# Performance work log

Measured on AMD Instinct MI355X. Metric: run time of the kernel, lower is better.

Reference implementation:

```python
import jax, jax.numpy as jnp
import numpy as np

N_NODES = 50000
N_EDGES = 800000
N_GRAPHS = 1000
IN_CH = 78
HID = 128
EPS = 1e-5


def _mean_aggr(x, src, dst, n):
    # scatter-mean of source-node features onto destination nodes
    s = jax.ops.segment_sum(x[src], dst, num_segments=n)
    deg = jax.ops.segment_sum(jnp.ones((src.shape[0],), x.dtype), dst, num_segments=n)
    return s / jnp.maximum(deg, 1.0)[:, None]


def _sage(x, src, dst, W_n, b_n, W_r):
    # PyG SAGEConv (mean): lin_l(mean_j x_j) + lin_r(x_i); lin_l has bias
    agg = _mean_aggr(x, src, dst, x.shape[0])
    return agg @ W_n + b_n + x @ W_r


def _bn(x, gamma, beta):
    # training-mode BatchNorm1d over node dimension (biased variance)
    mu = jnp.mean(x, axis=0)
    var = jnp.mean((x - mu) ** 2, axis=0)
    return (x - mu) * jax.lax.rsqrt(var + EPS) * gamma + beta


def setup_inputs() -> dict:
    key = jax.random.key(0)
    ks = jax.random.split(key, 20)
    d = {}
    d["x"] = jax.random.normal(ks[0], (N_NODES, IN_CH), dtype=jnp.float32)
    d["edge_index"] = jax.random.randint(ks[1], (2, N_EDGES), 0, N_NODES, dtype=jnp.int64)
    d["batch"] = jnp.sort(jax.random.randint(ks[2], (N_NODES,), 0, N_GRAPHS, dtype=jnp.int64))
    dims = [(IN_CH, HID), (HID, HID), (HID, HID)]
    for i, (di, do) in enumerate(dims):
        d[f"W_n{i}"] = jax.random.normal(ks[3 + 4 * i], (di, do), dtype=jnp.float32) * 0.05
        d[f"b{i}"] = jnp.zeros((do,), dtype=jnp.float32)
        d[f"W_r{i}"] = jax.random.normal(ks[4 + 4 * i], (di, do), dtype=jnp.float32) * 0.05
        d[f"g{i}"] = jnp.ones((do,), dtype=jnp.float32)
        d[f"be{i}"] = jnp.zeros((do,), dtype=jnp.float32)
    d["Wh1"] = jax.random.normal(ks[16], (HID, HID // 2), dtype=jnp.float32) * 0.05
    d["bh1"] = jnp.zeros((HID // 2,), dtype=jnp.float32)
    d["Wh2"] = jax.random.normal(ks[17], (HID // 2, 1), dtype=jnp.float32) * 0.05
    d["bh2"] = jnp.zeros((1,), dtype=jnp.float32)
    return d


def reference(x, edge_index, batch,
              W_n0, b0, W_r0, g0, be0,
              W_n1, b1, W_r1, g1, be1,
              W_n2, b2, W_r2, g2, be2,
              Wh1, bh1, Wh2, bh2):
    src, dst = edge_index[0], edge_index[1]
    layers = [(W_n0, b0, W_r0, g0, be0), (W_n1, b1, W_r1, g1, be1), (W_n2, b2, W_r2, g2, be2)]
    h = x
    for W_n, b_n, W_r, gamma, beta in layers:
        h = jax.nn.relu(_bn(_sage(h, src, dst, W_n, b_n, W_r), gamma, beta))
    # global mean pool per graph: [N_GRAPHS, HID]
    s = jax.ops.segment_sum(h, batch, num_segments=N_GRAPHS)
    cnt = jax.ops.segment_sum(jnp.ones((h.shape[0],), h.dtype), batch, num_segments=N_GRAPHS)
    pooled = s / jnp.maximum(cnt, 1.0)[:, None]
    return jax.nn.relu(pooled @ Wh1 + bh1) @ Wh2 + bh2
```

## Files before the change

kernel.cpp:

```cpp
#include <hip/hip_runtime.h>
#include <hip/hip_bf16.h>
#include <math.h>

#define HID 128
#define NSB 128
#define NBLK_BIN 256
#define BINC_CAP 6144

typedef short short8 __attribute__((ext_vector_type(8)));
typedef float f32x4 __attribute__((ext_vector_type(4)));

__global__ void prep_kernel(const float* __restrict__ x, float* __restrict__ xp,
                            int* __restrict__ bcnt, int nbuck16,
                            float* __restrict__ pstats, int npstats,
                            const float* __restrict__ Wn0, const float* __restrict__ Wr0,
                            const float* __restrict__ Wn1, const float* __restrict__ Wr1,
                            const float* __restrict__ Wn2, const float* __restrict__ Wr2,
                            unsigned short* __restrict__ B0h, unsigned short* __restrict__ B0l,
                            unsigned short* __restrict__ B1h, unsigned short* __restrict__ B1l,
                            unsigned short* __restrict__ B2h, unsigned short* __restrict__ B2l,
                            int N, int K0, int K0pad) {
    int i = blockIdx.x * blockDim.x + threadIdx.x;
    if (i < nbuck16) bcnt[i] = 0;
    if (i < npstats) pstats[i] = 0.f;
    if (i < N * K0pad) {
        int row = i / K0pad;
        int c = i - row * K0pad;
        xp[i] = (c < K0) ? x[(size_t)row * K0 + c] : 0.f;
    }
    int n0 = 256 * K0pad, n1 = 256 * HID;
    if (i < n0 + 2 * n1) {
        const float *Wn, *Wr;
        unsigned short *bh, *bl;
        int K, idx;
        if (i < n0) { Wn = Wn0; Wr = Wr0; bh = B0h; bl = B0l; K = K0; idx = i; }
        else if (i < n0 + n1) { Wn = Wn1; Wr = Wr1; bh = B1h; bl = B1l; K = HID; idx = i - n0; }
        else { Wn = Wn2; Wr = Wr2; bh = B2h; bl = B2l; K = HID; idx = i - n0 - n1; }
        int j = idx & 7;
        int lane = (idx >> 3) & 63;
        int cb = (idx >> 9) & 15;
        int ks = idx >> 13;
        int k = ks * 32 + ((lane >> 4) & 3) * 8 + j;
        int ch = 16 * cb + (lane & 15);
        float v = 0.f;
        if (k < K) v = (ch < 128) ? Wn[k * 128 + ch] : Wr[k * 128 + (ch - 128)];
        __hip_bfloat16 h = __float2bfloat16(v);
        float hf = __bfloat162float(h);
        __hip_bfloat16 l = __float2bfloat16(v - hf);
        bh[idx] = *(unsigned short*)&h;
        bl[idx] = *(unsigned short*)&l;
    }
}

__global__ void binA_kernel(const int* __restrict__ dst, int* __restrict__ bcnt,
                            int ne, int nbuck, int shift) {
    __shared__ int hist[512];
    int t = threadIdx.x;
    for (int i = t; i < 512; i += 256) hist[i] = 0;
    __syncthreads();
    size_t beg = (size_t)ne * blockIdx.x / NBLK_BIN;
    size_t end = (size_t)ne * (blockIdx.x + 1) / NBLK_BIN;
    for (size_t e = beg + t; e < end; e += 256)
        atomicAdd(&hist[dst[e] >> shift], 1);
    __syncthreads();
    for (int b = t; b < nbuck; b += 256) {
        int h = hist[b];
        if (h) atomicAdd(&bcnt[b * 16], h);
    }
}

__global__ __launch_bounds__(512) void bucket_scan_kernel(const int* __restrict__ bcnt,
                                                          int* __restrict__ bbase,
                                                          int* __restrict__ bcur, int nbuck) {
    __shared__ int tmp[512];
    int t = threadIdx.x;
    int v = (t < nbuck) ? bcnt[t * 16] : 0;
    tmp[t] = v;
    __syncthreads();
    for (int off = 1; off < 512; off <<= 1) {
        int u = 0;
        if (t >= off) u = tmp[t - off];
        __syncthreads();
        if (t >= off) tmp[t] += u;
        __syncthreads();
    }
    if (t < nbuck) {
        int exc = tmp[t] - v;
        bbase[t] = exc;
        bcur[t * 16] = exc;
        if (t == nbuck - 1) bbase[nbuck] = tmp[t];
    }
}

__global__ void binB_kernel(const int* __restrict__ src, const int* __restrict__ dst,
                            int* __restrict__ bcur, uint2* __restrict__ ebuf,
                            int ne, int nbuck, int shift) {
    __shared__ int hist[512];
    __shared__ int base[512];
    int t = threadIdx.x;
    for (int i = t; i < 512; i += 256) hist[i] = 0;
    __syncthreads();
    size_t beg = (size_t)ne * blockIdx.x / NBLK_BIN;
    size_t end = (size_t)ne * (blockIdx.x + 1) / NBLK_BIN;
    for (size_t e = beg + t; e < end; e += 256)
        atomicAdd(&hist[dst[e] >> shift], 1);
    __syncthreads();
    for (int b = t; b < nbuck; b += 256) {
        int h = hist[b];
        if (h) base[b] = atomicAdd(&bcur[b * 16], h);
        hist[b] = 0;
    }
    __syncthreads();
    for (size_t e = beg + t; e < end; e += 256) {
        int d = dst[e];
        int bk = d >> shift;
        int r = atomicAdd(&hist[bk], 1);
        ebuf[base[bk] + r] = make_uint2((unsigned)src[e], (unsigned)d);
    }
}

__global__ __launch_bounds__(512) void binC_kernel(const uint2* __restrict__ ebuf,
                                                   const int* __restrict__ bbase,
                                                   int* __restrict__ counts,
                                                   int* __restrict__ offsets,
                                                   int* __restrict__ esrc,
                                                   int N, int shift) {
    __shared__ int cnt[512], tmp[512], cur[512];
    __shared__ int sout[BINC_CAP];
    int b = blockIdx.x;
    int t = threadIdx.x;
    int node0 = b << shift;
    int npb = 1 << shift;
    if (node0 + npb > N) npb = N - node0;
    int ebase = bbase[b];
    int eend = bbase[b + 1];
    int total = eend - ebase;
    cnt[t] = 0;
    __syncthreads();
    for (int e = ebase + t; e < eend; e += 512)
        atomicAdd(&cnt[ebuf[e].y - node0], 1);
    __syncthreads();
    int v = cnt[t];
    tmp[t] = v;
    __syncthreads();
    for (int off = 1; off < 512; off <<= 1) {
        int u = 0;
        if (t >= off) u = tmp[t - off];
        __syncthreads();
        if (t >= off) tmp[t] += u;
        __syncthreads();
    }
    int exc = tmp[t] - v;
    cur[t] = exc;
    if (t < npb) {
        counts[node0 + t] = v;
        offsets[node0 + t] = ebase + exc;
    }
    __syncthreads();
    if (total <= BINC_CAP) {
        for (int e = ebase + t; e < eend; e += 512) {
            uint2 p = ebuf[e];
            int r = atomicAdd(&cur[(int)p.y - node0], 1);
            sout[r] = (int)p.x;
        }
        __syncthreads();
        for (int k = t; k < total; k += 512)
            esrc[ebase + k] = sout[k];
    } else {
        for (int e = ebase + t; e < eend; e += 512) {
            uint2 p = ebuf[e];
            int r = atomicAdd(&cur[(int)p.y - node0], 1);
            esrc[ebase + r] = (int)p.x;
        }
    }
}

template <int KPAD>
__global__ __launch_bounds__(256) void gemm_kernel(
    const float* __restrict__ A,
    const float* __restrict__ psum, const float* __restrict__ psumsq,
    const float* __restrict__ g, const float* __restrict__ be,
    const unsigned short* __restrict__ Bswh, const unsigned short* __restrict__ Bswl,
    unsigned short* __restrict__ U16, float* __restrict__ V, int N) {
    constexpr int LSTR = KPAD + 8;
    constexpr int KSTEPS = KPAD / 32;
    constexpr int ITERS = (32 * KPAD) / 1024;
    int tid = threadIdx.x;
    int lane = tid & 63;
    int w = tid >> 6;
    int q = lane >> 4;
    int m = lane & 15;
    int n0 = blockIdx.x * 32;
    int apply_bn = (psum != nullptr);

    __shared__ float s_sc[HID], s_sh[HID];
    __shared__ unsigned short sA_h[32 * LSTR], sA_l[32 * LSTR];
    if (apply_bn) {
        if (tid < HID) {
            double S = 0.0, Q = 0.0;
            for (int b = 0; b < NSB; b++) {
                S += (double)psum[b * HID + tid];
                Q += (double)psumsq[b * HID + tid];
            }
            double mu = S / (double)N;
            double var = Q / (double)N - mu * mu;
            if (var < 0.0) var = 0.0;
            float rs = (float)(1.0 / sqrt(var + 1e-5));
            float sc = g[tid] * rs;
            s_sc[tid] = sc;
            s_sh[tid] = be[tid] - (float)mu * sc;
        }
        __syncthreads();
    }

    float4 zreg[ITERS];
#pragma unroll
    for (int it = 0; it < ITERS; it++) {
        int idx = tid * 4 + it * 1024;
        int row = idx / KPAD;
        int col = idx - row * KPAD;
        int grow = n0 + row;
        if (grow >= N) grow = N - 1;
        zreg[it] = *(const float4*)(A + (size_t)grow * KPAD + col);
    }
#pragma unroll
    for (int it = 0; it < ITERS; it++) {
        int idx = tid * 4 + it * 1024;
        int row = idx / KPAD;
        int col = idx - row * KPAD;
        float y[4] = {zreg[it].x, zreg[it].y, zreg[it].z, zreg[it].w};
        if (apply_bn) {
#pragma unroll
            for (int j = 0; j < 4; j++)
                y[j] = fmaxf(fmaf(y[j], s_sc[col + j], s_sh[col + j]), 0.f);
        }
        ushort4 h4, l4;
        unsigned short* ph = (unsigned short*)&h4;
        unsigned short* pl = (unsigned short*)&l4;
#pragma unroll
        for (int j = 0; j < 4; j++) {
            __hip_bfloat16 h = __float2bfloat16(y[j]);
            float hf = __bfloat162float(h);
            __hip_bfloat16 lo = __float2bfloat16(y[j] - hf);
            ph[j] = *(unsigned short*)&h;
            pl[j] = *(unsigned short*)&lo;
        }
        *(ushort4*)&sA_h[row * LSTR + col] = h4;
        *(ushort4*)&sA_l[row * LSTR + col] = l4;
    }
    __syncthreads();

    f32x4 acc[2][4];
#pragma unroll
    for (int r = 0; r < 2; r++)
#pragma unroll
        for (int c = 0; c < 4; c++) acc[r][c] = (f32x4){0.f, 0.f, 0.f, 0.f};

#pragma unroll
    for (int ks = 0; ks < KSTEPS; ks++) {
        int ko = ks * 32 + q * 8;
        short8 ah[2], al[2], bh[4], bl[4];
#pragma unroll
        for (int c = 0; c < 4; c++) {
            int cb = 4 * w + c;
            size_t off = ((size_t)(ks * 16 + cb) * 64 + lane) * 8;
            bh[c] = __builtin_bit_cast(short8, *(const uint4*)(Bswh + off));
            bl[c] = __builtin_bit_cast(short8, *(const uint4*)(Bswl + off));
        }
#pragma unroll
        for (int r = 0; r < 2; r++) {
            int ao = (16 * r + m) * LSTR + ko;
            ah[r] = __builtin_bit_cast(short8, *(uint4*)&sA_h[ao]);
            al[r] = __builtin_bit_cast(short8, *(uint4*)&sA_l[ao]);
        }
#pragma unroll
        for (int r = 0; r < 2; r++)
#pragma unroll
            for (int c = 0; c < 4; c++) {
                acc[r][c] = __builtin_amdgcn_mfma_f32_16x16x32_bf16(ah[r], bh[c], acc[r][c], 0, 0, 0);
                acc[r][c] = __builtin_amdgcn_mfma_f32_16x16x32_bf16(ah[r], bl[c], acc[r][c], 0, 0, 0);
                acc[r][c] = __builtin_amdgcn_mfma_f32_16x16x32_bf16(al[r], bh[c], acc[r][c], 0, 0, 0);
            }
    }
    int colbase = (w & 1) * 64;
    if (w < 2) {
#pragma unroll
        for (int r = 0; r < 2; r++)
#pragma unroll
            for (int c = 0; c < 4; c++) {
                int col = colbase + 16 * c + m;
#pragma unroll
                for (int i = 0; i < 4; i++) {
                    int row = n0 + 16 * r + 4 * q + i;
                    if (row < N) {
                        __hip_bfloat16 h = __float2bfloat16(acc[r][c][i]);
                        U16[(size_t)row * HID + col] = *(unsigned short*)&h;
                    }
                }
            }
    } else {
#pragma unroll
        for (int r = 0; r < 2; r++)
#pragma unroll
            for (int c = 0; c < 4; c++) {
                int col = colbase + 16 * c + m;
#pragma unroll
                for (int i = 0; i < 4; i++) {
                    int row = n0 + 16 * r + 4 * q + i;
                    if (row < N) V[(size_t)row * HID + col] = acc[r][c][i];
                }
            }
    }
}

__global__ __launch_bounds__(256) void agg_kernel(const unsigned short* __restrict__ U16,
                                                  const float* __restrict__ V,
                                                  const float* __restrict__ bias,
                                                  const int* __restrict__ counts,
                                                  const int* __restrict__ offsets,
                                                  const int* __restrict__ esrc,
                                                  float* __restrict__ Z,
                                                  float* __restrict__ psum,
                                                  float* __restrict__ psumsq, int N) {
    int grp = threadIdx.x >> 5;
    int l32 = threadIdx.x & 31;
    int n = blockIdx.x * 8 + grp;
    bool valid = (n < N);
    f32x4 z = (f32x4){0.f, 0.f, 0.f, 0.f};

    if (valid) {
        int deg = counts[n];
        int st = offsets[n];
        int co = 4 * l32;

        auto cvt = [](uint2 raw) -> f32x4 {
            f32x4 v;
            v[0] = __uint_as_float(raw.x << 16);
            v[1] = __uint_as_float(raw.x & 0xffff0000u);
            v[2] = __uint_as_float(raw.y << 16);
            v[3] = __uint_as_float(raw.y & 0xffff0000u);
            return v;
        };

        f32x4 a0 = {0,0,0,0}, a1 = {0,0,0,0}, a2 = {0,0,0,0}, a3 = {0,0,0,0};
        f32x4 a4 = {0,0,0,0}, a5 = {0,0,0,0}, a6 = {0,0,0,0}, a7 = {0,0,0,0};
        int i = 0;
        for (; i + 7 < deg; i += 8) {
            int s0 = esrc[st + i + 0], s1 = esrc[st + i + 1];
            int s2 = esrc[st + i + 2], s3 = esrc[st + i + 3];
            int s4 = esrc[st + i + 4], s5 = esrc[st + i + 5];
            int s6 = esrc[st + i + 6], s7 = esrc[st + i + 7];
            uint2 r0 = *(const uint2*)(U16 + (size_t)s0 * HID + co);
            uint2 r1 = *(const uint2*)(U16 + (size_t)s1 * HID + co);
            uint2 r2 = *(const uint2*)(U16 + (size_t)s2 * HID + co);
            uint2 r3 = *(const uint2*)(U16 + (size_t)s3 * HID + co);
            uint2 r4 = *(const uint2*)(U16 + (size_t)s4 * HID + co);
            uint2 r5 = *(const uint2*)(U16 + (size_t)s5 * HID + co);
            uint2 r6 = *(const uint2*)(U16 + (size_t)s6 * HID + co);
            uint2 r7 = *(const uint2*)(U16 + (size_t)s7 * HID + co);
            a0 += cvt(r0); a1 += cvt(r1); a2 += cvt(r2); a3 += cvt(r3);
            a4 += cvt(r4); a5 += cvt(r5); a6 += cvt(r6); a7 += cvt(r7);
        }
        for (; i + 3 < deg; i += 4) {
            int s0 = esrc[st + i + 0], s1 = esrc[st + i + 1];
            int s2 = esrc[st + i + 2], s3 = esrc[st + i + 3];
            uint2 r0 = *(const uint2*)(U16 + (size_t)s0 * HID + co);
            uint2 r1 = *(const uint2*)(U16 + (size_t)s1 * HID + co);
            uint2 r2 = *(const uint2*)(U16 + (size_t)s2 * HID + co);
            uint2 r3 = *(const uint2*)(U16 + (size_t)s3 * HID + co);
            a0 += cvt(r0); a1 += cvt(r1); a2 += cvt(r2); a3 += cvt(r3);
        }
        for (; i < deg; i++) {
            uint2 r0 = *(const uint2*)(U16 + (size_t)esrc[st + i] * HID + co);
            a0 += cvt(r0);
        }
        f32x4 acc = ((a0 + a1) + (a2 + a3)) + ((a4 + a5) + (a6 + a7));
        float d = (float)(deg > 1 ? deg : 1);
        f32x4 vv = ((const f32x4*)V)[(size_t)n * 32 + l32];
        f32x4 bb = ((const f32x4*)bias)[l32];
        z = acc / d + vv + bb;
        ((f32x4*)Z)[(size_t)n * 32 + l32] = z;
    }

    __shared__ f32x4 bs[256], bq[256];
    int t = threadIdx.x;
    bs[t] = z;
    bq[t] = z * z;
    __syncthreads();
#pragma unroll
    for (int off = 4; off > 0; off >>= 1) {
        if (grp < off) {
            bs[t] += bs[t + off * 32];
            bq[t] += bq[t + off * 32];
        }
        __syncthreads();
    }
    if (grp == 0) {
        int slot = blockIdx.x & (NSB - 1);
        float* ps = psum + (size_t)slot * HID + 4 * l32;
        float* pq = psumsq + (size_t)slot * HID + 4 * l32;
        f32x4 s = bs[t];
        f32x4 qq = bq[t];
#pragma unroll
        for (int j = 0; j < 4; j++) {
            atomicAdd(&ps[j], s[j]);
            atomicAdd(&pq[j], qq[j]);
        }
    }
}

__global__ __launch_bounds__(128) void pool_head_kernel(const float* __restrict__ Z,
                                                        const float* __restrict__ psum,
                                                        const float* __restrict__ psumsq,
                                                        const float* __restrict__ g,
                                                        const float* __restrict__ be,
                                                        const int* __restrict__ batch,
                                                        const float* __restrict__ Wh1,
                                                        const float* __restrict__ bh1,
                                                        const float* __restrict__ Wh2,
                                                        const float* __restrict__ bh2,
                                                        float* __restrict__ out, int N) {
    int gph = blockIdx.x;
    __shared__ int bounds[2];
    __shared__ float p[128];
    int t = threadIdx.x;
    if (t < 2) {
        int target = gph + t;
        int lo = 0, hi = N;
        while (lo < hi) {
            int mid = (lo + hi) >> 1;
            if (batch[mid] < target) lo = mid + 1;
            else hi = mid;
        }
        bounds[t] = lo;
    }
    double S = 0.0, Q = 0.0;
    for (int b = 0; b < NSB; b++) {
        S += (double)psum[b * HID + t];
        Q += (double)psumsq[b * HID + t];
    }
    double mu = S / (double)N;
    double var = Q / (double)N - mu * mu;
    if (var < 0.0) var = 0.0;
    float rs = (float)(1.0 / sqrt(var + 1e-5));
    float sc = g[t] * rs;
    float sh = be[t] - (float)mu * sc;
    __syncthreads();
    int start = bounds[0], end = bounds[1];
    float s = 0.f;
    for (int n = start; n < end; n++)
        s += fmaxf(fmaf(Z[(size_t)n * HID + t], sc, sh), 0.f);
    p[t] = s / fmaxf((float)(end - start), 1.f);
    __syncthreads();
    if (t < 64) {
        float acc = bh1[t];
        for (int k = 0; k < 128; k++) acc = fmaf(p[k], Wh1[k * 64 + t], acc);
        acc = fmaxf(acc, 0.f);
        float prod = acc * Wh2[t];
        for (int off = 32; off > 0; off >>= 1) prod += __shfl_down(prod, off);
        if (t == 0) out[gph] = prod + bh2[0];
    }
}

extern "C" void kernel_launch(void* const* d_in, const int* in_sizes, int n_in,
                              void* d_out, int out_size, void* d_ws, size_t ws_size,
                              hipStream_t stream) {
    const float* x = (const float*)d_in[0];
    const int* ei = (const int*)d_in[1];
    const int* batch = (const int*)d_in[2];
    const float* Wn[3] = {(const float*)d_in[3], (const float*)d_in[8], (const float*)d_in[13]};
    const float* bb[3] = {(const float*)d_in[4], (const float*)d_in[9], (const float*)d_in[14]};
    const float* Wr[3] = {(const float*)d_in[5], (const float*)d_in[10], (const float*)d_in[15]};
    const float* gg[3] = {(const float*)d_in[6], (const float*)d_in[11], (const float*)d_in[16]};
    const float* be[3] = {(const float*)d_in[7], (const float*)d_in[12], (const float*)d_in[17]};
    const float* Wh1 = (const float*)d_in[18];
    const float* bh1 = (const float*)d_in[19];
    const float* Wh2 = (const float*)d_in[20];
    const float* bh2 = (const float*)d_in[21];
    float* out = (float*)d_out;

    const int N = in_sizes[2];
    const int NE = in_sizes[1] / 2;
    const int NG = out_size;
    const int K0 = in_sizes[0] / N;
    const int K0pad = (K0 <= 96) ? 96 : 128;

    const int* src = ei;
    const int* dst = ei + NE;

    int shift = 7;
    int nbuck = (N + 127) >> 7;
    while (nbuck > 512) { shift++; nbuck = (N + (1 << shift) - 1) >> shift; }

    char* w = (char*)d_ws;
    auto alloc = [&](size_t bytes) -> void* {
        void* p = (void*)w;
        w += (bytes + 255) & ~(size_t)255;
        return p;
    };
    unsigned short* bufU16 = (unsigned short*)alloc((size_t)N * HID * 2);
    float* bufV = (float*)alloc((size_t)N * HID * 4);
    float* bufZ = (float*)alloc((size_t)N * HID * 4);
    float* xp = (float*)alloc((size_t)N * K0pad * 4);
    unsigned short* BTh[3];
    unsigned short* BTl[3];
    BTh[0] = (unsigned short*)alloc((size_t)256 * K0pad * 2);
    BTl[0] = (unsigned short*)alloc((size_t)256 * K0pad * 2);
    BTh[1] = (unsigned short*)alloc((size_t)256 * HID * 2);
    BTl[1] = (unsigned short*)alloc((size_t)256 * HID * 2);
    BTh[2] = (unsigned short*)alloc((size_t)256 * HID * 2);
    BTl[2] = (unsigned short*)alloc((size_t)256 * HID * 2);
    int* counts = (int*)alloc((size_t)N * 4);
    int* offsets = (int*)alloc((size_t)(N + 1) * 4);
    int* esrc = (int*)alloc((size_t)NE * 4);
    int* bcnt = (int*)alloc((size_t)512 * 16 * 4);
    int* bcur = (int*)alloc((size_t)512 * 16 * 4);
    int* bbase = (int*)alloc((size_t)(512 + 1) * 4);
    float* pstats = (float*)alloc((size_t)3 * 2 * NSB * HID * 4);
    uint2* ebuf = (uint2*)bufZ;
    (void)ws_size;
    (void)n_in;

    const int npstats = 3 * 2 * NSB * HID;

    size_t prep_total = (size_t)N * K0pad;
    prep_kernel<<<(prep_total + 255) / 256, 256, 0, stream>>>(
        x, xp, bcnt, nbuck * 16, pstats, npstats,
        Wn[0], Wr[0], Wn[1], Wr[1], Wn[2], Wr[2],
        BTh[0], BTl[0], BTh[1], BTl[1], BTh[2], BTl[2], N, K0, K0pad);

    binA_kernel<<<NBLK_BIN, 256, 0, stream>>>(dst, bcnt, NE, nbuck, shift);
    bucket_scan_kernel<<<1, 512, 0, stream>>>(bcnt, bbase, bcur, nbuck);
    binB_kernel<<<NBLK_BIN, 256, 0, stream>>>(src, dst, bcur, ebuf, NE, nbuck, shift);
    binC_kernel<<<nbuck, 512, 0, stream>>>(ebuf, bbase, counts, offsets, esrc, N, shift);

    int gblocks = (N + 31) / 32;
    int ablocks = (N + 7) / 8;
    for (int l = 0; l < 3; l++) {
        const float* Ain = (l == 0) ? xp : bufZ;
        int Kpad = (l == 0) ? K0pad : HID;
        const float* ppsum = (l == 0) ? (const float*)nullptr : pstats + (size_t)(l - 1) * 2 * NSB * HID;
        const float* ppsq = (l == 0) ? (const float*)nullptr : pstats + (size_t)(l - 1) * 2 * NSB * HID + NSB * HID;
        const float* pg = (l == 0) ? (const float*)nullptr : gg[l - 1];
        const float* pb = (l == 0) ? (const float*)nullptr : be[l - 1];
        if (Kpad == 96)
            gemm_kernel<96><<<gblocks, 256, 0, stream>>>(Ain, ppsum, ppsq, pg, pb,
                                                         BTh[l], BTl[l], bufU16, bufV, N);
        else
            gemm_kernel<128><<<gblocks, 256, 0, stream>>>(Ain, ppsum, ppsq, pg, pb,
                                                          BTh[l], BTl[l], bufU16, bufV, N);
        agg_kernel<<<ablocks, 256, 0, stream>>>(bufU16, bufV, bb[l], counts, offsets, esrc, bufZ,
                                                pstats + (size_t)l * 2 * NSB * HID,
                                                pstats + (size_t)l * 2 * NSB * HID + NSB * HID, N);
    }

    pool_head_kernel<<<NG, 128, 0, stream>>>(bufZ,
                                             pstats + (size_t)2 * 2 * NSB * HID,
                                             pstats + (size_t)2 * 2 * NSB * HID + NSB * HID,
                                             gg[2], be[2], batch, Wh1, bh1, Wh2, bh2, out, N);
}
```

Before: 402.7 us.

## Restructure aggregation to one wave per node with 16-byte gathers

The mean-aggregation kernel now assigns one 64-lane wave per destination node, with four quarter-waves each handling different edges and 16 lanes covering the 128 bf16 features via 16-byte loads. Partial sums are combined with cross-lane shuffles, and the BatchNorm statistics reduction is simplified to a single shared-memory pass. The aim is wider memory transactions and more edges in flight per node, reducing gather latency. In exchange, each block covers fewer nodes, so the grid doubles in size, and the shuffle reduction adds a little overhead.

```diff
diff --git a/kernel.cpp b/kernel.cpp
--- a/kernel.cpp
+++ b/kernel.cpp
@@ -322,89 +322,93 @@
                                                   float* __restrict__ Z,
                                                   float* __restrict__ psum,
                                                   float* __restrict__ psumsq, int N) {
-    int grp = threadIdx.x >> 5;
-    int l32 = threadIdx.x & 31;
-    int n = blockIdx.x * 8 + grp;
-    bool valid = (n < N);
-    f32x4 z = (f32x4){0.f, 0.f, 0.f, 0.f};
-
-    if (valid) {
+    int wv = threadIdx.x >> 6;
+    int lane = threadIdx.x & 63;
+    int q = lane >> 4;
+    int l16 = lane & 15;
+    int n = blockIdx.x * 4 + wv;
+    int co = 8 * l16;
+
+    auto cvtlo = [](unsigned u) -> float { return __uint_as_float(u << 16); };
+    auto cvthi = [](unsigned u) -> float { return __uint_as_float(u & 0xffff0000u); };
+
+    f32x4 zL = {0.f, 0.f, 0.f, 0.f}, zH = {0.f, 0.f, 0.f, 0.f};
+    if (n < N) {
         int deg = counts[n];
         int st = offsets[n];
-        int co = 4 * l32;
-
-        auto cvt = [](uint2 raw) -> f32x4 {
-            f32x4 v;
-            v[0] = __uint_as_float(raw.x << 16);
-            v[1] = __uint_as_float(raw.x & 0xffff0000u);
-            v[2] = __uint_as_float(raw.y << 16);
-            v[3] = __uint_as_float(raw.y & 0xffff0000u);
-            return v;
-        };
-
-        f32x4 a0 = {0,0,0,0}, a1 = {0,0,0,0}, a2 = {0,0,0,0}, a3 = {0,0,0,0};
-        f32x4 a4 = {0,0,0,0}, a5 = {0,0,0,0}, a6 = {0,0,0,0}, a7 = {0,0,0,0};
+        f32x4 aL0 = {0,0,0,0}, aH0 = {0,0,0,0}, aL1 = {0,0,0,0}, aH1 = {0,0,0,0};
         int i = 0;
         for (; i + 7 < deg; i += 8) {
-            int s0 = esrc[st + i + 0], s1 = esrc[st + i + 1];
-            int s2 = esrc[st + i + 2], s3 = esrc[st + i + 3];
-            int s4 = esrc[st + i + 4], s5 = esrc[st + i + 5];
-            int s6 = esrc[st + i + 6], s7 = esrc[st + i + 7];
-            uint2 r0 = *(const uint2*)(U16 + (size_t)s0 * HID + co);
-            uint2 r1 = *(const uint2*)(U16 + (size_t)s1 * HID + co);
-            uint2 r2 = *(const uint2*)(U16 + (size_t)s2 * HID + co);
-            uint2 r3 = *(const uint2*)(U16 + (size_t)s3 * HID + co);
-            uint2 r4 = *(const uint2*)(U16 + (size_t)s4 * HID + co);
-            uint2 r5 = *(const uint2*)(U16 + (size_t)s5 * HID + co);
-            uint2 r6 = *(const uint2*)(U16 + (size_t)s6 * HID + co);
-            uint2 r7 = *(const uint2*)(U16 + (size_t)s7 * HID + co);
-            a0 += cvt(r0); a1 += cvt(r1); a2 += cvt(r2); a3 += cvt(r3);
-            a4 += cvt(r4); a5 += cvt(r5); a6 += cvt(r6); a7 += cvt(r7);
+            int s0 = esrc[st + i + q];
+            int s1 = esrc[st + i + 4 + q];
+            uint4 r0 = *(const uint4*)(U16 + (size_t)s0 * HID + co);
+            uint4 r1 = *(const uint4*)(U16 + (size_t)s1 * HID + co);
+            aL0[0] += cvtlo(r0.x); aL0[1] += cvthi(r0.x);
+            aL0[2] += cvtlo(r0.y); aL0[3] += cvthi(r0.y);
+            aH0[0] += cvtlo(r0.z); aH0[1] += cvthi(r0.z);
+            aH0[2] += cvtlo(r0.w); aH0[3] += cvthi(r0.w);
+            aL1[0] += cvtlo(r1.x); aL1[1] += cvthi(r1.x);
+            aL1[2] += cvtlo(r1.y); aL1[3] += cvthi(r1.y);
+            aH1[0] += cvtlo(r1.z); aH1[1] += cvthi(r1.z);
+            aH1[2] += cvtlo(r1.w); aH1[3] += cvthi(r1.w);
         }
         for (; i + 3 < deg; i += 4) {
-            int s0 = esrc[st + i + 0], s1 = esrc[st + i + 1];
-            int s2 = esrc[st + i + 2], s3 = esrc[st + i + 3];
-            uint2 r0 = *(const uint2*)(U16 + (size_t)s0 * HID + co);
-            uint2 r1 = *(const uint2*)(U16 + (size_t)s1 * HID + co);
-            uint2 r2 = *(const uint2*)(U16 + (size_t)s2 * HID + co);
-            uint2 r3 = *(const uint2*)(U16 + (size_t)s3 * HID + co);
-            a0 += cvt(r0); a1 += cvt(r1); a2 += cvt(r2); a3 += cvt(r3);
-        }
-        for (; i < deg; i++) {
-            uint2 r0 = *(const uint2*)(U16 + (size_t)esrc[st + i] * HID + co);
-            a0 += cvt(r0);
-        }
-        f32x4 acc = ((a0 + a1) + (a2 + a3)) + ((a4 + a5) + (a6 + a7));
-        float d = (float)(deg > 1 ? deg : 1);
-        f32x4 vv = ((const f32x4*)V)[(size_t)n * 32 + l32];
-        f32x4 bb = ((const f32x4*)bias)[l32];
-        z = acc / d + vv + bb;
-        ((f32x4*)Z)[(size_t)n * 32 + l32] = z;
-    }
-
-    __shared__ f32x4 bs[256], bq[256];
+            int s0 = esrc[st + i + q];
+            uint4 r0 = *(const uint4*)(U16 + (size_t)s0 * HID + co);
+            aL0[0] += cvtlo(r0.x); aL0[1] += cvthi(r0.x);
+            aL0[2] += cvtlo(r0.y); aL0[3] += cvthi(r0.y);
+            aH0[0] += cvtlo(r0.z); aH0[1] += cvthi(r0.z);
+            aH0[2] += cvtlo(r0.w); aH0[3] += cvthi(r0.w);
+        }
+        if (i + q < deg) {
+            int s1 = esrc[st + i + q];
+            uint4 r1 = *(const uint4*)(U16 + (size_t)s1 * HID + co);
+            aL1[0] += cvtlo(r1.x); aL1[1] += cvthi(r1.x);
+            aL1[2] += cvtlo(r1.y); aL1[3] += cvthi(r1.y);
+            aH1[0] += cvtlo(r1.z); aH1[1] += cvthi(r1.z);
+            aH1[2] += cvtlo(r1.w); aH1[3] += cvthi(r1.w);
+        }
+        f32x4 aL = aL0 + aL1;
+        f32x4 aH = aH0 + aH1;
+#pragma unroll
+        for (int j = 0; j < 4; j++) {
+            aL[j] += __shfl_down(aL[j], 32);
+            aL[j] += __shfl_down(aL[j], 16);
+            aH[j] += __shfl_down(aH[j], 32);
+            aH[j] += __shfl_down(aH[j], 16);
+        }
+        if (lane < 16) {
+            float d = (float)(deg > 1 ? deg : 1);
+            const f32x4* V4 = (const f32x4*)V;
+            const f32x4* B4 = (const f32x4*)bias;
+            zL = aL / d + V4[(size_t)n * 32 + 2 * l16] + B4[2 * l16];
+            zH = aH / d + V4[(size_t)n * 32 + 2 * l16 + 1] + B4[2 * l16 + 1];
+            ((f32x4*)Z)[(size_t)n * 32 + 2 * l16] = zL;
+            ((f32x4*)Z)[(size_t)n * 32 + 2 * l16 + 1] = zH;
+        }
+    }
+
+    __shared__ f32x4 bsL[4][16], bsH[4][16], bqL[4][16], bqH[4][16];
+    if (lane < 16) {
+        bsL[wv][l16] = zL; bsH[wv][l16] = zH;
+        bqL[wv][l16] = zL * zL; bqH[wv][l16] = zH * zH;
+    }
+    __syncthreads();
     int t = threadIdx.x;
-    bs[t] = z;
-    bq[t] = z * z;
-    __syncthreads();
-#pragma unroll
-    for (int off = 4; off > 0; off >>= 1) {
-        if (grp < off) {
-            bs[t] += bs[t + off * 32];
-            bq[t] += bq[t + off * 32];
-        }
-        __syncthreads();
-    }
-    if (grp == 0) {
+    if (t < 16) {
+        f32x4 sL = (bsL[0][t] + bsL[1][t]) + (bsL[2][t] + bsL[3][t]);
+        f32x4 sH = (bsH[0][t] + bsH[1][t]) + (bsH[2][t] + bsH[3][t]);
+        f32x4 qL = (bqL[0][t] + bqL[1][t]) + (bqL[2][t] + bqL[3][t]);
+        f32x4 qH = (bqH[0][t] + bqH[1][t]) + (bqH[2][t] + bqH[3][t]);
         int slot = blockIdx.x & (NSB - 1);
-        float* ps = psum + (size_t)slot * HID + 4 * l32;
-        float* pq = psumsq + (size_t)slot * HID + 4 * l32;
-        f32x4 s = bs[t];
-        f32x4 qq = bq[t];
+        float* ps = psum + (size_t)slot * HID + 8 * t;
+        float* pq = psumsq + (size_t)slot * HID + 8 * t;
 #pragma unroll
         for (int j = 0; j < 4; j++) {
-            atomicAdd(&ps[j], s[j]);
-            atomicAdd(&pq[j], qq[j]);
+            atomicAdd(&ps[j], sL[j]);
+            atomicAdd(&ps[4 + j], sH[j]);
+            atomicAdd(&pq[j], qL[j]);
+            atomicAdd(&pq[4 + j], qH[j]);
         }
     }
 }
@@ -535,7 +539,7 @@
     binC_kernel<<<nbuck, 512, 0, stream>>>(ebuf, bbase, counts, offsets, esrc, N, shift);
 
     int gblocks = (N + 31) / 32;
-    int ablocks = (N + 7) / 8;
+    int ablocks = (N + 3) / 4;
     for (int l = 0; l < 3; l++) {
         const float* Ain = (l == 0) ? xp : bufZ;
         int Kpad = (l == 0) ? K0pad : HID;
```

Result: slower. 565.1 us (+40.3%).
